# Kernel optimization log

Hardware: AMD Instinct MI355X
Metric: run time of the kernel (lower is better)

The kernel has to match this reference:

```python
import jax, jax.numpy as jnp
import numpy as np

NEAR_PLANE = 1e-4
MIN_COV = 1e-4
SIGMA_RADIUS = 3.0
ALPHA_MAX = 0.999  # clamp for numerical stability of log1p(-alpha)


def setup_inputs() -> dict:
    key = jax.random.key(0)
    k1, k2, k3, k4, k5 = jax.random.split(key, 5)
    N = 1024
    H = W = 192
    # Gaussians in front of an identity-pose camera
    xy = jax.random.uniform(k1, (N, 2), minval=-2.0, maxval=2.0)
    z = jax.random.uniform(k2, (N, 1), minval=1.0, maxval=8.0)
    means = jnp.concatenate([xy, z], axis=1).astype(jnp.float32)
    A = jax.random.normal(k3, (N, 3, 3), dtype=jnp.float32) * 0.05
    covariances = jnp.einsum('nij,nkj->nik', A, A) + 1e-4 * jnp.eye(3, dtype=jnp.float32)
    colors = jax.random.uniform(k4, (N, 3), dtype=jnp.float32)
    opacities = jax.random.uniform(k5, (N,), dtype=jnp.float32)
    fx = fy = 200.0
    intrinsics = jnp.array([[fx, 0.0, W / 2.0], [0.0, fy, H / 2.0], [0.0, 0.0, 1.0]], dtype=jnp.float32)
    camera_to_world = jnp.eye(4, dtype=jnp.float32)
    return {
        'means': means, 'covariances': covariances, 'colors': colors,
        'opacities': opacities, 'intrinsics': intrinsics,
        'camera_to_world': camera_to_world, 'height': H, 'width': W,
    }


def _render(means, covariances, colors, opacities, intrinsics, camera_to_world, height, width):
    # world -> camera
    R = camera_to_world[:3, :3].T                      # rotation_w2c
    t = -R @ camera_to_world[:3, 3]
    mc = means @ R.T + t                               # [N,3] camera-space means
    covc = jnp.einsum('ij,njk,lk->nil', R, covariances, R)  # [N,3,3]
    x, y, z = mc[:, 0], mc[:, 1], mc[:, 2]
    vis = z > NEAR_PLANE
    sz = jnp.where(vis, z, 1.0)
    fx, fy = intrinsics[0, 0], intrinsics[1, 1]
    cx, cy = intrinsics[0, 2], intrinsics[1, 2]
    mx = fx * x / sz + cx
    my = fy * y / sz + cy
    # projection Jacobian [N,2,3]
    zer = jnp.zeros_like(sz)
    J = jnp.stack([
        jnp.stack([fx / sz, zer, -fx * x / (sz * sz)], axis=-1),
        jnp.stack([zer, fy / sz, -fy * y / (sz * sz)], axis=-1),
    ], axis=1)
    cov2 = jnp.einsum('nij,njk,nlk->nil', J, covc, J) + MIN_COV * jnp.eye(2, dtype=means.dtype)
    a, b, c = cov2[:, 0, 0], cov2[:, 0, 1], cov2[:, 1, 1]
    # max eigenvalue -> support radius -> axis-aligned bbox
    disc = jnp.sqrt(jnp.clip((a - c) ** 2 + 4.0 * b * b, 0.0, None))
    lam = jnp.maximum(0.5 * (a + c + disc), MIN_COV)
    rad = SIGMA_RADIUS * jnp.sqrt(lam)
    min_x = jnp.floor(mx - rad); max_x = jnp.ceil(mx + rad)
    min_y = jnp.floor(my - rad); max_y = jnp.ceil(my + rad)
    overlap = vis & (max_x >= 0) & (min_x < width) & (max_y >= 0) & (min_y < height)
    # depth sort (culled Gaussians pushed to the back with alpha forced to 0)
    order = jnp.argsort(jnp.where(overlap, z, jnp.inf))
    mx, my = mx[order], my[order]
    a, b, c = a[order], b[order], c[order]
    min_x, max_x = min_x[order], max_x[order]
    min_y, max_y = min_y[order], max_y[order]
    op = jnp.where(overlap[order], opacities[order], 0.0)
    cols = colors[order]
    # inverse 2x2 covariance
    det = jnp.maximum(a * c - b * b, 1e-12)
    ia, ib, ic = c / det, -b / det, a / det
    xs = jnp.arange(width, dtype=mx.dtype)
    ys = jnp.arange(height, dtype=mx.dtype)
    dx = xs[None, None, :] - mx[:, None, None]         # [N,1,W]
    dy = ys[None, :, None] - my[:, None, None]         # [N,H,1]
    # Mahalanobis distance per (gaussian, pixel): [N,H,W]
    q = (ia[:, None, None] * dx * dx
         + 2.0 * ib[:, None, None] * dx * dy
         + ic[:, None, None] * dy * dy)
    w = jnp.exp(-0.5 * q)
    in_x = (xs[None, None, :] >= min_x[:, None, None]) & (xs[None, None, :] <= max_x[:, None, None])
    in_y = (ys[None, :, None] >= min_y[:, None, None]) & (ys[None, :, None] <= max_y[:, None, None])
    inside = (in_x & in_y).astype(w.dtype)
    alpha = jnp.clip(op[:, None, None] * w, 0.0, ALPHA_MAX) * inside  # [N,H,W]
    # front-to-back compositing: T_i = prod_{j<i}(1 - alpha_j), exclusive
    logc = jnp.cumsum(jnp.log1p(-alpha), axis=0)
    T = jnp.exp(jnp.concatenate([jnp.zeros_like(logc[:1]), logc[:-1]], axis=0))
    img = jnp.einsum('nhw,nc->hwc', alpha * T, cols)   # [H,W,3]
    return img


def reference(means, covariances, colors, opacities, intrinsics, camera_to_world, height, width):
    return _render(means, covariances, colors, opacities, intrinsics, camera_to_world, height, width)
```

## Files before the change

kernel.cpp:

```cpp
#include <hip/hip_runtime.h>
#include <stdint.h>
#include <math.h>

#define NEAR_PLANE 0.0001f
#define MIN_COV    0.0001f
#define SIGMA_RAD  3.0f
#define ALPHA_MAX  0.999f


__global__ __launch_bounds__(256) void gs_prep(
        const float* __restrict__ means,
        const float* __restrict__ covs,
        const float* __restrict__ colors,
        const float* __restrict__ opac,
        const float* __restrict__ K,
        const float* __restrict__ c2w,
        const int* __restrict__ hp, const int* __restrict__ wp,
        float4* __restrict__ params,
        unsigned* __restrict__ zb,
        uint2* __restrict__ bbox,
        int N) {
    int i = blockIdx.x * blockDim.x + threadIdx.x;
    if (i >= N) return;
    float Wf = (float)(*wp), Hf = (float)(*hp);

    float R[3][3];
    #pragma unroll
    for (int r = 0; r < 3; ++r)
        #pragma unroll
        for (int c = 0; c < 3; ++c)
            R[r][c] = c2w[c * 4 + r];
    float ct0 = c2w[3], ct1 = c2w[7], ct2 = c2w[11];
    float t0 = -(R[0][0]*ct0 + R[0][1]*ct1 + R[0][2]*ct2);
    float t1 = -(R[1][0]*ct0 + R[1][1]*ct1 + R[1][2]*ct2);
    float t2 = -(R[2][0]*ct0 + R[2][1]*ct1 + R[2][2]*ct2);

    float m0 = means[i*3+0], m1 = means[i*3+1], m2 = means[i*3+2];
    float x = R[0][0]*m0 + R[0][1]*m1 + R[0][2]*m2 + t0;
    float y = R[1][0]*m0 + R[1][1]*m1 + R[1][2]*m2 + t1;
    float z = R[2][0]*m0 + R[2][1]*m1 + R[2][2]*m2 + t2;

    const float* C = covs + i * 9;
    float M[3][3], CC[3][3];
    #pragma unroll
    for (int r = 0; r < 3; ++r)
        #pragma unroll
        for (int c = 0; c < 3; ++c)
            M[r][c] = R[r][0]*C[0*3+c] + R[r][1]*C[1*3+c] + R[r][2]*C[2*3+c];
    #pragma unroll
    for (int r = 0; r < 3; ++r)
        #pragma unroll
        for (int c = 0; c < 3; ++c)
            CC[r][c] = M[r][0]*R[c][0] + M[r][1]*R[c][1] + M[r][2]*R[c][2];

    bool vis = z > NEAR_PLANE;
    float sz = vis ? z : 1.0f;
    float fx = K[0], fy = K[4], cx = K[2], cy = K[5];
    float mx = fx * x / sz + cx;
    float my = fy * y / sz + cy;

    float a0 = fx / sz, a2 = -fx * x / (sz * sz);
    float b1 = fy / sz, b2 = -fy * y / (sz * sz);
    float u0 = a0*CC[0][0] + a2*CC[2][0];
    float u1 = a0*CC[0][1] + a2*CC[2][1];
    float u2 = a0*CC[0][2] + a2*CC[2][2];
    float v1 = b1*CC[1][1] + b2*CC[2][1];
    float v2 = b1*CC[1][2] + b2*CC[2][2];
    float a = u0*a0 + u2*a2 + MIN_COV;
    float b = u1*b1 + u2*b2;
    float c = v1*b1 + v2*b2 + MIN_COV;

    float disc = sqrtf(fmaxf((a - c)*(a - c) + 4.0f*b*b, 0.0f));
    float lam  = fmaxf(0.5f*(a + c + disc), MIN_COV);
    float rad  = SIGMA_RAD * sqrtf(lam);
    float minx = floorf(mx - rad), maxx = ceilf(mx + rad);
    float miny = floorf(my - rad), maxy = ceilf(my + rad);
    bool overlap = vis && (maxx >= 0.0f) && (minx < Wf) && (maxy >= 0.0f) && (miny < Hf);

    float det = fmaxf(a*c - b*b, 1e-12f);

    int mnx, mxx, mny, mxy;
    if (overlap) {
        mnx = (int)fmaxf(fminf(minx,  32767.0f), -32768.0f);
        mxx = (int)fmaxf(fminf(maxx,  32767.0f), -32768.0f);
        mny = (int)fmaxf(fminf(miny,  32767.0f), -32768.0f);
        mxy = (int)fmaxf(fminf(maxy,  32767.0f), -32768.0f);
    } else {
        mnx = 32767; mxx = -32768; mny = 32767; mxy = -32768;
    }
    float op = overlap ? opac[i] : 0.0f;
    params[i*3+0] = make_float4(mx, my, c / det, -b / det);
    params[i*3+1] = make_float4(a / det, op, colors[i*3+0], colors[i*3+1]);
    params[i*3+2] = make_float4(colors[i*3+2], 0.0f, 0.0f, 0.0f);

    zb[i] = overlap ? __float_as_uint(z) : 0x7F800000u;
    bbox[i] = make_uint2((unsigned)(mnx & 0xFFFF) | ((unsigned)(mxx & 0xFFFF) << 16),
                         (unsigned)(mny & 0xFFFF) | ((unsigned)(mxy & 0xFFFF) << 16));
}

__global__ __launch_bounds__(256) void gs_render(
        const float4* __restrict__ params,
        const unsigned* __restrict__ zb,
        const uint2* __restrict__ bbox,
        int W, int H, int N,
        float* __restrict__ out) {
    __shared__ unsigned long long sk[1024];
    __shared__ float4 sp[1024 * 3];
    __shared__ float4 s_part[4][64];
    __shared__ int s_cnt;

    int tid = threadIdx.x;
    int lane = tid & 63, wv = tid >> 6;
    int tilesX = (W + 7) >> 3;
    int tile = blockIdx.x;
    int tx0 = (tile % tilesX) << 3, ty0 = (tile / tilesX) << 3;
    int txMax = tx0 + 7, tyMax = ty0 + 7;

    if (tid == 0) s_cnt = 0;
    __syncthreads();

    for (int r = 0; r < N; r += 256) {
        int i = r + tid;
        bool keep = false;
        unsigned long long key = 0;
        if (i < N) {
            uint2 bb = bbox[i];
            int gmnx = ((int)bb.x << 16) >> 16, gmxx = (int)bb.x >> 16;
            int gmny = ((int)bb.y << 16) >> 16, gmxy = (int)bb.y >> 16;
            keep = (gmxx >= tx0) & (gmnx <= txMax) & (gmxy >= ty0) & (gmny <= tyMax);
            if (keep) key = ((unsigned long long)zb[i] << 32) | (unsigned)i;
        }
        unsigned long long m = __ballot(keep);
        int base = 0;
        if (lane == 0 && m) base = atomicAdd(&s_cnt, __popcll(m));
        base = __shfl(base, 0, 64);
        if (keep) {
            int pos = __popcll(m & ((1ull << lane) - 1ull));
            sk[base + pos] = key;
        }
    }
    __syncthreads();
    int S = s_cnt;

    int pad = 1;
    while (pad < S) pad <<= 1;
    for (int i = S + tid; i < pad; i += 256) sk[i] = ~0ull;
    __syncthreads();
    for (int k = 2; k <= pad; k <<= 1) {
        for (int j = k >> 1; j > 0; j >>= 1) {
            for (int i = tid; i < pad; i += 256) {
                int ixj = i ^ j;
                if (ixj > i) {
                    unsigned long long A = sk[i], B = sk[ixj];
                    bool up = (i & k) == 0;
                    if ((A > B) == up) { sk[i] = B; sk[ixj] = A; }
                }
            }
            __syncthreads();
        }
    }

    for (int i = tid; i < S; i += 256) {
        int g = (int)(sk[i] & 0xFFFFFFFFull);
        sp[i*3+0] = params[g*3+0];
        sp[i*3+1] = params[g*3+1];
        sp[i*3+2] = params[g*3+2];
    }
    __syncthreads();

    int per = (S + 3) >> 2;
    int lo = wv * per, hi = min(S, lo + per);
    int px = tx0 + (lane & 7), py = ty0 + (lane >> 3);
    float fpx = (float)px, fpy = (float)py;
    float T = 1.0f, accr = 0.0f, accg = 0.0f, accb = 0.0f;
    for (int i = lo; i < hi; ++i) {
        float4 l0 = sp[i*3+0];
        float4 l1 = sp[i*3+1];
        float  cb = sp[i*3+2].x;
        float dx = fpx - l0.x, dy = fpy - l0.y;
        float q = fmaf(l0.z * dx, dx, fmaf(2.0f * l0.w * dx, dy, l1.x * dy * dy));
        float w = __expf(-0.5f * q);
        float alpha = fminf(l1.y * w, ALPHA_MAX);
        float at = alpha * T;
        accr = fmaf(at, l1.z, accr);
        accg = fmaf(at, l1.w, accg);
        accb = fmaf(at, cb, accb);
        T = T - at;
        if (__all(T < 1e-6f)) break;
    }
    s_part[wv][lane] = make_float4(accr, accg, accb, T);
    __syncthreads();

    if (wv == 0 && px < W && py < H) {
        float Tc = 1.0f, r = 0.0f, g = 0.0f, b = 0.0f;
        #pragma unroll
        for (int s = 0; s < 4; ++s) {
            float4 p = s_part[s][lane];
            r = fmaf(Tc, p.x, r);
            g = fmaf(Tc, p.y, g);
            b = fmaf(Tc, p.z, b);
            Tc *= p.w;
        }
        int pix = py * W + px;
        out[pix*3+0] = r;
        out[pix*3+1] = g;
        out[pix*3+2] = b;
    }
}

extern "C" void kernel_launch(void* const* d_in, const int* in_sizes, int n_in,
                              void* d_out, int out_size, void* d_ws, size_t ws_size,
                              hipStream_t stream) {
    const float* means  = (const float*)d_in[0];
    const float* covs   = (const float*)d_in[1];
    const float* colors = (const float*)d_in[2];
    const float* opac   = (const float*)d_in[3];
    const float* K      = (const float*)d_in[4];
    const float* c2w    = (const float*)d_in[5];
    const int*   hp     = (const int*)d_in[6];
    const int*   wp     = (const int*)d_in[7];

    int N = in_sizes[0] / 3;
    int npix = out_size / 3;
    int W = (int)(sqrt((double)npix) + 0.5);
    int H = npix / W;

    char* ws = (char*)d_ws;
    float4*   params = (float4*)ws;
    unsigned* zbp    = (unsigned*)(ws + (size_t)N * 48);
    uint2*    bboxp  = (uint2*)(ws + (size_t)N * 52);

    gs_prep<<<(N + 255) / 256, 256, 0, stream>>>(means, covs, colors, opac, K, c2w,
                                                 hp, wp, params, zbp, bboxp, N);

    int tilesX = (W + 7) / 8, tilesY = (H + 7) / 8;
    gs_render<<<tilesX * tilesY, 256, 0, stream>>>(params, zbp, bboxp, W, H, N,
                                                   (float*)d_out);
}
```

Before: 23.77 us.

## Fuse projection into per-tile render kernel and sort small lists in registers

```diff
diff --git a/kernel.cpp b/kernel.cpp
--- a/kernel.cpp
+++ b/kernel.cpp
@@ -7,23 +7,39 @@
 #define SIGMA_RAD  3.0f
 #define ALPHA_MAX  0.999f
 
-
-__global__ __launch_bounds__(256) void gs_prep(
+__device__ inline unsigned long long shflx64(unsigned long long v, int j) {
+    int lo = __shfl_xor((int)(unsigned)(v & 0xFFFFFFFFull), j, 64);
+    int hi = __shfl_xor((int)(unsigned)(v >> 32), j, 64);
+    return ((unsigned long long)(unsigned)hi << 32) | (unsigned)lo;
+}
+
+__global__ __launch_bounds__(256) void gs_fused(
         const float* __restrict__ means,
         const float* __restrict__ covs,
         const float* __restrict__ colors,
         const float* __restrict__ opac,
         const float* __restrict__ K,
         const float* __restrict__ c2w,
-        const int* __restrict__ hp, const int* __restrict__ wp,
-        float4* __restrict__ params,
-        unsigned* __restrict__ zb,
-        uint2* __restrict__ bbox,
-        int N) {
-    int i = blockIdx.x * blockDim.x + threadIdx.x;
-    if (i >= N) return;
-    float Wf = (float)(*wp), Hf = (float)(*hp);
-
+        int W, int H, int N,
+        float* __restrict__ out) {
+    __shared__ float4 sp[1024 * 3];
+    __shared__ unsigned long long sk[1024];
+    __shared__ float4 s_aux[256];
+    __shared__ int s_cnt;
+
+    unsigned* szb = (unsigned*)s_aux;
+    float4 (*s_part)[64] = (float4 (*)[64])s_aux;
+
+    int tid = threadIdx.x;
+    int lane = tid & 63, wv = tid >> 6;
+    int tilesX = (W + 7) >> 3;
+    int tile = blockIdx.x;
+    int tx0 = (tile % tilesX) << 3, ty0 = (tile / tilesX) << 3;
+    int txMax = tx0 + 7, tyMax = ty0 + 7;
+
+    if (tid == 0) s_cnt = 0;
+
+    float Wf = (float)W, Hf = (float)H;
     float R[3][3];
     #pragma unroll
     for (int r = 0; r < 3; ++r)
@@ -34,101 +50,85 @@
     float t0 = -(R[0][0]*ct0 + R[0][1]*ct1 + R[0][2]*ct2);
     float t1 = -(R[1][0]*ct0 + R[1][1]*ct1 + R[1][2]*ct2);
     float t2 = -(R[2][0]*ct0 + R[2][1]*ct1 + R[2][2]*ct2);
-
-    float m0 = means[i*3+0], m1 = means[i*3+1], m2 = means[i*3+2];
-    float x = R[0][0]*m0 + R[0][1]*m1 + R[0][2]*m2 + t0;
-    float y = R[1][0]*m0 + R[1][1]*m1 + R[1][2]*m2 + t1;
-    float z = R[2][0]*m0 + R[2][1]*m1 + R[2][2]*m2 + t2;
-
-    const float* C = covs + i * 9;
-    float M[3][3], CC[3][3];
-    #pragma unroll
-    for (int r = 0; r < 3; ++r)
-        #pragma unroll
-        for (int c = 0; c < 3; ++c)
-            M[r][c] = R[r][0]*C[0*3+c] + R[r][1]*C[1*3+c] + R[r][2]*C[2*3+c];
-    #pragma unroll
-    for (int r = 0; r < 3; ++r)
-        #pragma unroll
-        for (int c = 0; c < 3; ++c)
-            CC[r][c] = M[r][0]*R[c][0] + M[r][1]*R[c][1] + M[r][2]*R[c][2];
-
-    bool vis = z > NEAR_PLANE;
-    float sz = vis ? z : 1.0f;
     float fx = K[0], fy = K[4], cx = K[2], cy = K[5];
-    float mx = fx * x / sz + cx;
-    float my = fy * y / sz + cy;
-
-    float a0 = fx / sz, a2 = -fx * x / (sz * sz);
-    float b1 = fy / sz, b2 = -fy * y / (sz * sz);
-    float u0 = a0*CC[0][0] + a2*CC[2][0];
-    float u1 = a0*CC[0][1] + a2*CC[2][1];
-    float u2 = a0*CC[0][2] + a2*CC[2][2];
-    float v1 = b1*CC[1][1] + b2*CC[2][1];
-    float v2 = b1*CC[1][2] + b2*CC[2][2];
-    float a = u0*a0 + u2*a2 + MIN_COV;
-    float b = u1*b1 + u2*b2;
-    float c = v1*b1 + v2*b2 + MIN_COV;
-
-    float disc = sqrtf(fmaxf((a - c)*(a - c) + 4.0f*b*b, 0.0f));
-    float lam  = fmaxf(0.5f*(a + c + disc), MIN_COV);
-    float rad  = SIGMA_RAD * sqrtf(lam);
-    float minx = floorf(mx - rad), maxx = ceilf(mx + rad);
-    float miny = floorf(my - rad), maxy = ceilf(my + rad);
-    bool overlap = vis && (maxx >= 0.0f) && (minx < Wf) && (maxy >= 0.0f) && (miny < Hf);
-
-    float det = fmaxf(a*c - b*b, 1e-12f);
-
-    int mnx, mxx, mny, mxy;
-    if (overlap) {
-        mnx = (int)fmaxf(fminf(minx,  32767.0f), -32768.0f);
-        mxx = (int)fmaxf(fminf(maxx,  32767.0f), -32768.0f);
-        mny = (int)fmaxf(fminf(miny,  32767.0f), -32768.0f);
-        mxy = (int)fmaxf(fminf(maxy,  32767.0f), -32768.0f);
-    } else {
-        mnx = 32767; mxx = -32768; mny = 32767; mxy = -32768;
-    }
-    float op = overlap ? opac[i] : 0.0f;
-    params[i*3+0] = make_float4(mx, my, c / det, -b / det);
-    params[i*3+1] = make_float4(a / det, op, colors[i*3+0], colors[i*3+1]);
-    params[i*3+2] = make_float4(colors[i*3+2], 0.0f, 0.0f, 0.0f);
-
-    zb[i] = overlap ? __float_as_uint(z) : 0x7F800000u;
-    bbox[i] = make_uint2((unsigned)(mnx & 0xFFFF) | ((unsigned)(mxx & 0xFFFF) << 16),
-                         (unsigned)(mny & 0xFFFF) | ((unsigned)(mxy & 0xFFFF) << 16));
-}
-
-__global__ __launch_bounds__(256) void gs_render(
-        const float4* __restrict__ params,
-        const unsigned* __restrict__ zb,
-        const uint2* __restrict__ bbox,
-        int W, int H, int N,
-        float* __restrict__ out) {
-    __shared__ unsigned long long sk[1024];
-    __shared__ float4 sp[1024 * 3];
-    __shared__ float4 s_part[4][64];
-    __shared__ int s_cnt;
-
-    int tid = threadIdx.x;
-    int lane = tid & 63, wv = tid >> 6;
-    int tilesX = (W + 7) >> 3;
-    int tile = blockIdx.x;
-    int tx0 = (tile % tilesX) << 3, ty0 = (tile / tilesX) << 3;
-    int txMax = tx0 + 7, tyMax = ty0 + 7;
-
-    if (tid == 0) s_cnt = 0;
-    __syncthreads();
-
-    for (int r = 0; r < N; r += 256) {
-        int i = r + tid;
+
+    #pragma unroll 4
+    for (int i = tid; i < N; i += 256) {
+        float m0 = means[i*3+0], m1 = means[i*3+1], m2 = means[i*3+2];
+        float x = R[0][0]*m0 + R[0][1]*m1 + R[0][2]*m2 + t0;
+        float y = R[1][0]*m0 + R[1][1]*m1 + R[1][2]*m2 + t1;
+        float z = R[2][0]*m0 + R[2][1]*m1 + R[2][2]*m2 + t2;
+
+        const float* C = covs + i * 9;
+        float M[3][3], CC[3][3];
+        #pragma unroll
+        for (int r = 0; r < 3; ++r)
+            #pragma unroll
+            for (int c = 0; c < 3; ++c)
+                M[r][c] = R[r][0]*C[0*3+c] + R[r][1]*C[1*3+c] + R[r][2]*C[2*3+c];
+        #pragma unroll
+        for (int r = 0; r < 3; ++r)
+            #pragma unroll
+            for (int c = 0; c < 3; ++c)
+                CC[r][c] = M[r][0]*R[c][0] + M[r][1]*R[c][1] + M[r][2]*R[c][2];
+
+        bool vis = z > NEAR_PLANE;
+        float sz = vis ? z : 1.0f;
+        float mx = fx * x / sz + cx;
+        float my = fy * y / sz + cy;
+
+        float a0 = fx / sz, a2 = -fx * x / (sz * sz);
+        float b1 = fy / sz, b2 = -fy * y / (sz * sz);
+        float u0 = a0*CC[0][0] + a2*CC[2][0];
+        float u1 = a0*CC[0][1] + a2*CC[2][1];
+        float u2 = a0*CC[0][2] + a2*CC[2][2];
+        float v1 = b1*CC[1][1] + b2*CC[2][1];
+        float v2 = b1*CC[1][2] + b2*CC[2][2];
+        float a = u0*a0 + u2*a2 + MIN_COV;
+        float b = u1*b1 + u2*b2;
+        float c = v1*b1 + v2*b2 + MIN_COV;
+
+        float disc = sqrtf(fmaxf((a - c)*(a - c) + 4.0f*b*b, 0.0f));
+        float lam  = fmaxf(0.5f*(a + c + disc), MIN_COV);
+        float rad  = SIGMA_RAD * sqrtf(lam);
+        float minx = floorf(mx - rad), maxx = ceilf(mx + rad);
+        float miny = floorf(my - rad), maxy = ceilf(my + rad);
+        bool overlap = vis && (maxx >= 0.0f) && (minx < Wf) && (maxy >= 0.0f) && (miny < Hf);
+
+        float det = fmaxf(a*c - b*b, 1e-12f);
+
+        int mnx, mxx, mny, mxy;
+        if (overlap) {
+            mnx = (int)fmaxf(fminf(minx,  32767.0f), -32768.0f);
+            mxx = (int)fmaxf(fminf(maxx,  32767.0f), -32768.0f);
+            mny = (int)fmaxf(fminf(miny,  32767.0f), -32768.0f);
+            mxy = (int)fmaxf(fminf(maxy,  32767.0f), -32768.0f);
+        } else {
+            mnx = 32767; mxx = -32768; mny = 32767; mxy = -32768;
+        }
+        unsigned p01 = (unsigned)(mnx & 0xFFFF) | ((unsigned)(mxx & 0xFFFF) << 16);
+        unsigned p23 = (unsigned)(mny & 0xFFFF) | ((unsigned)(mxy & 0xFFFF) << 16);
+        float op = overlap ? opac[i] : 0.0f;
+
+        sp[i*3+0] = make_float4(mx, my, c / det, -b / det);
+        sp[i*3+1] = make_float4(a / det, op, colors[i*3+0], colors[i*3+1]);
+        sp[i*3+2] = make_float4(__int_as_float((int)p01), __int_as_float((int)p23),
+                                colors[i*3+2], 0.0f);
+        szb[i] = overlap ? __float_as_uint(z) : 0x7F800000u;
+    }
+    __syncthreads();
+
+    for (int rr = 0; rr < N; rr += 256) {
+        int i = rr + tid;
         bool keep = false;
         unsigned long long key = 0;
         if (i < N) {
-            uint2 bb = bbox[i];
-            int gmnx = ((int)bb.x << 16) >> 16, gmxx = (int)bb.x >> 16;
-            int gmny = ((int)bb.y << 16) >> 16, gmxy = (int)bb.y >> 16;
+            float4 v2r = sp[i*3+2];
+            int bb01 = __float_as_int(v2r.x), bb23 = __float_as_int(v2r.y);
+            int gmnx = (bb01 << 16) >> 16, gmxx = bb01 >> 16;
+            int gmny = (bb23 << 16) >> 16, gmxy = bb23 >> 16;
             keep = (gmxx >= tx0) & (gmnx <= txMax) & (gmxy >= ty0) & (gmny <= tyMax);
-            if (keep) key = ((unsigned long long)zb[i] << 32) | (unsigned)i;
+            if (keep) key = ((unsigned long long)szb[i] << 32) | (unsigned)i;
         }
         unsigned long long m = __ballot(keep);
         int base = 0;
@@ -144,29 +144,47 @@
 
     int pad = 1;
     while (pad < S) pad <<= 1;
-    for (int i = S + tid; i < pad; i += 256) sk[i] = ~0ull;
-    __syncthreads();
-    for (int k = 2; k <= pad; k <<= 1) {
-        for (int j = k >> 1; j > 0; j >>= 1) {
-            for (int i = tid; i < pad; i += 256) {
-                int ixj = i ^ j;
-                if (ixj > i) {
-                    unsigned long long A = sk[i], B = sk[ixj];
-                    bool up = (i & k) == 0;
-                    if ((A > B) == up) { sk[i] = B; sk[ixj] = A; }
+
+    if (pad <= 256) {
+        int v = tid;
+        unsigned long long key = (v < S) ? sk[v] : ~0ull;
+        for (int k = 2; k <= pad; k <<= 1) {
+            for (int j = k >> 1; j > 0; j >>= 1) {
+                if (j >= 64) {
+                    if (v < pad) sk[v] = key;
+                    __syncthreads();
+                    unsigned long long p = (v < pad) ? sk[v ^ j] : 0;
+                    __syncthreads();
+                    if (v < pad) {
+                        bool tm = (((v & j) == 0) == ((v & k) == 0));
+                        key = (tm == (key < p)) ? key : p;
+                    }
+                } else {
+                    unsigned long long p = shflx64(key, j);
+                    bool tm = (((v & j) == 0) == ((v & k) == 0));
+                    key = (tm == (key < p)) ? key : p;
                 }
             }
-            __syncthreads();
-        }
-    }
-
-    for (int i = tid; i < S; i += 256) {
-        int g = (int)(sk[i] & 0xFFFFFFFFull);
-        sp[i*3+0] = params[g*3+0];
-        sp[i*3+1] = params[g*3+1];
-        sp[i*3+2] = params[g*3+2];
-    }
-    __syncthreads();
+        }
+        if (v < pad) sk[v] = key;
+        __syncthreads();
+    } else {
+        for (int i = S + tid; i < pad; i += 256) sk[i] = ~0ull;
+        __syncthreads();
+        for (int k = 2; k <= pad; k <<= 1) {
+            for (int j = k >> 1; j > 0; j >>= 1) {
+                for (int i = tid; i < pad; i += 256) {
+                    int ixj = i ^ j;
+                    if (ixj > i) {
+                        unsigned long long A = sk[i], B = sk[ixj];
+                        bool up = (i & k) == 0;
+                        if ((A > B) == up) { sk[i] = B; sk[ixj] = A; }
+                    }
+                }
+                __syncthreads();
+            }
+        }
+    }
 
     int per = (S + 3) >> 2;
     int lo = wv * per, hi = min(S, lo + per);
@@ -174,20 +192,25 @@
     float fpx = (float)px, fpy = (float)py;
     float T = 1.0f, accr = 0.0f, accg = 0.0f, accb = 0.0f;
     for (int i = lo; i < hi; ++i) {
-        float4 l0 = sp[i*3+0];
-        float4 l1 = sp[i*3+1];
-        float  cb = sp[i*3+2].x;
+        int g = (int)(sk[i] & 0xFFFFFFFFull);
+        float4 l0 = sp[g*3+0];
+        float4 l1 = sp[g*3+1];
+        float4 l2 = sp[g*3+2];
+        int b01 = __float_as_int(l2.x), b23 = __float_as_int(l2.y);
+        bool inside = (px >= ((b01 << 16) >> 16)) & (px <= (b01 >> 16))
+                    & (py >= ((b23 << 16) >> 16)) & (py <= (b23 >> 16));
         float dx = fpx - l0.x, dy = fpy - l0.y;
         float q = fmaf(l0.z * dx, dx, fmaf(2.0f * l0.w * dx, dy, l1.x * dy * dy));
         float w = __expf(-0.5f * q);
-        float alpha = fminf(l1.y * w, ALPHA_MAX);
+        float alpha = inside ? fminf(l1.y * w, ALPHA_MAX) : 0.0f;
         float at = alpha * T;
         accr = fmaf(at, l1.z, accr);
         accg = fmaf(at, l1.w, accg);
-        accb = fmaf(at, cb, accb);
+        accb = fmaf(at, l2.z, accb);
         T = T - at;
         if (__all(T < 1e-6f)) break;
     }
+    __syncthreads();
     s_part[wv][lane] = make_float4(accr, accg, accb, T);
     __syncthreads();
 
@@ -217,23 +240,13 @@
     const float* opac   = (const float*)d_in[3];
     const float* K      = (const float*)d_in[4];
     const float* c2w    = (const float*)d_in[5];
-    const int*   hp     = (const int*)d_in[6];
-    const int*   wp     = (const int*)d_in[7];
 
     int N = in_sizes[0] / 3;
     int npix = out_size / 3;
     int W = (int)(sqrt((double)npix) + 0.5);
     int H = npix / W;
 
-    char* ws = (char*)d_ws;
-    float4*   params = (float4*)ws;
-    unsigned* zbp    = (unsigned*)(ws + (size_t)N * 48);
-    uint2*    bboxp  = (uint2*)(ws + (size_t)N * 52);
-
-    gs_prep<<<(N + 255) / 256, 256, 0, stream>>>(means, covs, colors, opac, K, c2w,
-                                                 hp, wp, params, zbp, bboxp, N);
-
     int tilesX = (W + 7) / 8, tilesY = (H + 7) / 8;
-    gs_render<<<tilesX * tilesY, 256, 0, stream>>>(params, zbp, bboxp, W, H, N,
-                                                   (float*)d_out);
+    gs_fused<<<tilesX * tilesY, 256, 0, stream>>>(means, covs, colors, opac, K, c2w,
+                                                  W, H, N, (float*)d_out);
 }
```

After: 23.89 us. About the same (+0.5%).

## Sort gaussians once globally by depth instead of per-tile bitonic sort

Applied to the files above, without the earlier changes.

```diff
diff --git a/kernel.cpp b/kernel.cpp
--- a/kernel.cpp
+++ b/kernel.cpp
@@ -7,6 +7,11 @@
 #define SIGMA_RAD  3.0f
 #define ALPHA_MAX  0.999f
 
+__device__ inline unsigned long long shflx64(unsigned long long v, int j) {
+    int lo = __shfl_xor((int)(unsigned)(v & 0xFFFFFFFFull), j, 64);
+    int hi = __shfl_xor((int)(unsigned)(v >> 32), j, 64);
+    return ((unsigned long long)(unsigned)hi << 32) | (unsigned)lo;
+}
 
 __global__ __launch_bounds__(256) void gs_prep(
         const float* __restrict__ means,
@@ -88,26 +93,52 @@
     } else {
         mnx = 32767; mxx = -32768; mny = 32767; mxy = -32768;
     }
+    unsigned p01 = (unsigned)(mnx & 0xFFFF) | ((unsigned)(mxx & 0xFFFF) << 16);
+    unsigned p23 = (unsigned)(mny & 0xFFFF) | ((unsigned)(mxy & 0xFFFF) << 16);
     float op = overlap ? opac[i] : 0.0f;
+
     params[i*3+0] = make_float4(mx, my, c / det, -b / det);
     params[i*3+1] = make_float4(a / det, op, colors[i*3+0], colors[i*3+1]);
-    params[i*3+2] = make_float4(colors[i*3+2], 0.0f, 0.0f, 0.0f);
-
+    params[i*3+2] = make_float4(__int_as_float((int)p01), __int_as_float((int)p23),
+                                colors[i*3+2], 0.0f);
     zb[i] = overlap ? __float_as_uint(z) : 0x7F800000u;
-    bbox[i] = make_uint2((unsigned)(mnx & 0xFFFF) | ((unsigned)(mxx & 0xFFFF) << 16),
-                         (unsigned)(mny & 0xFFFF) | ((unsigned)(mxy & 0xFFFF) << 16));
+    bbox[i] = make_uint2(p01, p23);
+}
+
+__global__ __launch_bounds__(1024) void gs_sort(
+        const unsigned* __restrict__ zb,
+        int* __restrict__ perm, int N) {
+    __shared__ unsigned long long sk[1024];
+    int i = threadIdx.x;
+    unsigned long long key = ((unsigned long long)zb[i] << 32) | (unsigned)i;
+    for (int k = 2; k <= N; k <<= 1) {
+        int j = k >> 1;
+        for (; j >= 64; j >>= 1) {
+            sk[i] = key;
+            __syncthreads();
+            unsigned long long p = sk[i ^ j];
+            __syncthreads();
+            bool tm = (((i & j) == 0) == ((i & k) == 0));
+            key = (tm == (key < p)) ? key : p;
+        }
+        for (; j >= 1; j >>= 1) {
+            unsigned long long p = shflx64(key, j);
+            bool tm = (((i & j) == 0) == ((i & k) == 0));
+            key = (tm == (key < p)) ? key : p;
+        }
+    }
+    perm[i] = (int)(key & 0xFFFFFFFFull);
 }
 
 __global__ __launch_bounds__(256) void gs_render(
         const float4* __restrict__ params,
-        const unsigned* __restrict__ zb,
         const uint2* __restrict__ bbox,
+        const int* __restrict__ perm,
         int W, int H, int N,
         float* __restrict__ out) {
-    __shared__ unsigned long long sk[1024];
-    __shared__ float4 sp[1024 * 3];
+    __shared__ int s_surv[1024];
+    __shared__ int s_wcnt[4];
     __shared__ float4 s_part[4][64];
-    __shared__ int s_cnt;
 
     int tid = threadIdx.x;
     int lane = tid & 63, wv = tid >> 6;
@@ -116,75 +147,58 @@
     int tx0 = (tile % tilesX) << 3, ty0 = (tile / tilesX) << 3;
     int txMax = tx0 + 7, tyMax = ty0 + 7;
 
-    if (tid == 0) s_cnt = 0;
-    __syncthreads();
-
-    for (int r = 0; r < N; r += 256) {
-        int i = r + tid;
+    int running = 0;
+    for (int rr = 0; rr < N; rr += 256) {
+        int i = rr + tid;
         bool keep = false;
-        unsigned long long key = 0;
+        int g = 0;
         if (i < N) {
-            uint2 bb = bbox[i];
+            g = perm[i];
+            uint2 bb = bbox[g];
             int gmnx = ((int)bb.x << 16) >> 16, gmxx = (int)bb.x >> 16;
             int gmny = ((int)bb.y << 16) >> 16, gmxy = (int)bb.y >> 16;
             keep = (gmxx >= tx0) & (gmnx <= txMax) & (gmxy >= ty0) & (gmny <= tyMax);
-            if (keep) key = ((unsigned long long)zb[i] << 32) | (unsigned)i;
         }
         unsigned long long m = __ballot(keep);
-        int base = 0;
-        if (lane == 0 && m) base = atomicAdd(&s_cnt, __popcll(m));
-        base = __shfl(base, 0, 64);
+        if (lane == 0) s_wcnt[wv] = __popcll(m);
+        __syncthreads();
+        int base = running;
+        #pragma unroll
+        for (int w = 0; w < 4; ++w) {
+            int cw = s_wcnt[w];
+            if (w < wv) base += cw;
+            running += cw;
+        }
         if (keep) {
             int pos = __popcll(m & ((1ull << lane) - 1ull));
-            sk[base + pos] = key;
-        }
-    }
-    __syncthreads();
-    int S = s_cnt;
-
-    int pad = 1;
-    while (pad < S) pad <<= 1;
-    for (int i = S + tid; i < pad; i += 256) sk[i] = ~0ull;
-    __syncthreads();
-    for (int k = 2; k <= pad; k <<= 1) {
-        for (int j = k >> 1; j > 0; j >>= 1) {
-            for (int i = tid; i < pad; i += 256) {
-                int ixj = i ^ j;
-                if (ixj > i) {
-                    unsigned long long A = sk[i], B = sk[ixj];
-                    bool up = (i & k) == 0;
-                    if ((A > B) == up) { sk[i] = B; sk[ixj] = A; }
-                }
-            }
-            __syncthreads();
-        }
-    }
-
-    for (int i = tid; i < S; i += 256) {
-        int g = (int)(sk[i] & 0xFFFFFFFFull);
-        sp[i*3+0] = params[g*3+0];
-        sp[i*3+1] = params[g*3+1];
-        sp[i*3+2] = params[g*3+2];
-    }
-    __syncthreads();
+            s_surv[base + pos] = g;
+        }
+        __syncthreads();
+    }
+    int S = running;
 
     int per = (S + 3) >> 2;
     int lo = wv * per, hi = min(S, lo + per);
     int px = tx0 + (lane & 7), py = ty0 + (lane >> 3);
     float fpx = (float)px, fpy = (float)py;
     float T = 1.0f, accr = 0.0f, accg = 0.0f, accb = 0.0f;
+    #pragma unroll 2
     for (int i = lo; i < hi; ++i) {
-        float4 l0 = sp[i*3+0];
-        float4 l1 = sp[i*3+1];
-        float  cb = sp[i*3+2].x;
+        int g = s_surv[i];
+        float4 l0 = params[g*3+0];
+        float4 l1 = params[g*3+1];
+        float4 l2 = params[g*3+2];
+        int b01 = __float_as_int(l2.x), b23 = __float_as_int(l2.y);
+        bool inside = (px >= ((b01 << 16) >> 16)) & (px <= (b01 >> 16))
+                    & (py >= ((b23 << 16) >> 16)) & (py <= (b23 >> 16));
         float dx = fpx - l0.x, dy = fpy - l0.y;
         float q = fmaf(l0.z * dx, dx, fmaf(2.0f * l0.w * dx, dy, l1.x * dy * dy));
         float w = __expf(-0.5f * q);
-        float alpha = fminf(l1.y * w, ALPHA_MAX);
+        float alpha = inside ? fminf(l1.y * w, ALPHA_MAX) : 0.0f;
         float at = alpha * T;
         accr = fmaf(at, l1.z, accr);
         accg = fmaf(at, l1.w, accg);
-        accb = fmaf(at, cb, accb);
+        accb = fmaf(at, l2.z, accb);
         T = T - at;
         if (__all(T < 1e-6f)) break;
     }
@@ -229,11 +243,13 @@
     float4*   params = (float4*)ws;
     unsigned* zbp    = (unsigned*)(ws + (size_t)N * 48);
     uint2*    bboxp  = (uint2*)(ws + (size_t)N * 52);
+    int*      perm   = (int*)(ws + (size_t)N * 60);
 
     gs_prep<<<(N + 255) / 256, 256, 0, stream>>>(means, covs, colors, opac, K, c2w,
                                                  hp, wp, params, zbp, bboxp, N);
+    gs_sort<<<1, N, 0, stream>>>(zbp, perm, N);
 
     int tilesX = (W + 7) / 8, tilesY = (H + 7) / 8;
-    gs_render<<<tilesX * tilesY, 256, 0, stream>>>(params, zbp, bboxp, W, H, N,
+    gs_render<<<tilesX * tilesY, 256, 0, stream>>>(params, bboxp, perm, W, H, N,
                                                    (float*)d_out);
 }
```

New measurement: 26.27 us. +10.5%, slower.

## Use register bitonic sort with shuffles and read params directly from global memory

Applied to the files above, without the earlier changes.

```diff
diff --git a/kernel.cpp b/kernel.cpp
--- a/kernel.cpp
+++ b/kernel.cpp
@@ -7,6 +7,11 @@
 #define SIGMA_RAD  3.0f
 #define ALPHA_MAX  0.999f
 
+__device__ inline unsigned long long shflx64(unsigned long long v, int j) {
+    int lo = __shfl_xor((int)(unsigned)(v & 0xFFFFFFFFull), j, 64);
+    int hi = __shfl_xor((int)(unsigned)(v >> 32), j, 64);
+    return ((unsigned long long)(unsigned)hi << 32) | (unsigned)lo;
+}
 
 __global__ __launch_bounds__(256) void gs_prep(
         const float* __restrict__ means,
@@ -88,14 +93,16 @@
     } else {
         mnx = 32767; mxx = -32768; mny = 32767; mxy = -32768;
     }
+    unsigned p01 = (unsigned)(mnx & 0xFFFF) | ((unsigned)(mxx & 0xFFFF) << 16);
+    unsigned p23 = (unsigned)(mny & 0xFFFF) | ((unsigned)(mxy & 0xFFFF) << 16);
     float op = overlap ? opac[i] : 0.0f;
+
     params[i*3+0] = make_float4(mx, my, c / det, -b / det);
     params[i*3+1] = make_float4(a / det, op, colors[i*3+0], colors[i*3+1]);
-    params[i*3+2] = make_float4(colors[i*3+2], 0.0f, 0.0f, 0.0f);
-
+    params[i*3+2] = make_float4(__int_as_float((int)p01), __int_as_float((int)p23),
+                                colors[i*3+2], 0.0f);
     zb[i] = overlap ? __float_as_uint(z) : 0x7F800000u;
-    bbox[i] = make_uint2((unsigned)(mnx & 0xFFFF) | ((unsigned)(mxx & 0xFFFF) << 16),
-                         (unsigned)(mny & 0xFFFF) | ((unsigned)(mxy & 0xFFFF) << 16));
+    bbox[i] = make_uint2(p01, p23);
 }
 
 __global__ __launch_bounds__(256) void gs_render(
@@ -105,7 +112,6 @@
         int W, int H, int N,
         float* __restrict__ out) {
     __shared__ unsigned long long sk[1024];
-    __shared__ float4 sp[1024 * 3];
     __shared__ float4 s_part[4][64];
     __shared__ int s_cnt;
 
@@ -119,8 +125,8 @@
     if (tid == 0) s_cnt = 0;
     __syncthreads();
 
-    for (int r = 0; r < N; r += 256) {
-        int i = r + tid;
+    for (int rr = 0; rr < N; rr += 256) {
+        int i = rr + tid;
         bool keep = false;
         unsigned long long key = 0;
         if (i < N) {
@@ -144,47 +150,70 @@
 
     int pad = 1;
     while (pad < S) pad <<= 1;
-    for (int i = S + tid; i < pad; i += 256) sk[i] = ~0ull;
-    __syncthreads();
-    for (int k = 2; k <= pad; k <<= 1) {
-        for (int j = k >> 1; j > 0; j >>= 1) {
-            for (int i = tid; i < pad; i += 256) {
-                int ixj = i ^ j;
-                if (ixj > i) {
-                    unsigned long long A = sk[i], B = sk[ixj];
-                    bool up = (i & k) == 0;
-                    if ((A > B) == up) { sk[i] = B; sk[ixj] = A; }
+
+    if (pad <= 256) {
+        int v = tid;
+        unsigned long long key = (v < S) ? sk[v] : ~0ull;
+        for (int k = 2; k <= pad; k <<= 1) {
+            for (int j = k >> 1; j > 0; j >>= 1) {
+                if (j >= 64) {
+                    if (v < pad) sk[v] = key;
+                    __syncthreads();
+                    unsigned long long p = (v < pad) ? sk[v ^ j] : 0;
+                    __syncthreads();
+                    if (v < pad) {
+                        bool tm = (((v & j) == 0) == ((v & k) == 0));
+                        key = (tm == (key < p)) ? key : p;
+                    }
+                } else {
+                    unsigned long long p = shflx64(key, j);
+                    bool tm = (((v & j) == 0) == ((v & k) == 0));
+                    key = (tm == (key < p)) ? key : p;
                 }
             }
-            __syncthreads();
-        }
-    }
-
-    for (int i = tid; i < S; i += 256) {
-        int g = (int)(sk[i] & 0xFFFFFFFFull);
-        sp[i*3+0] = params[g*3+0];
-        sp[i*3+1] = params[g*3+1];
-        sp[i*3+2] = params[g*3+2];
-    }
-    __syncthreads();
+        }
+        if (v < pad) sk[v] = key;
+        __syncthreads();
+    } else {
+        for (int i = S + tid; i < pad; i += 256) sk[i] = ~0ull;
+        __syncthreads();
+        for (int k = 2; k <= pad; k <<= 1) {
+            for (int j = k >> 1; j > 0; j >>= 1) {
+                for (int i = tid; i < pad; i += 256) {
+                    int ixj = i ^ j;
+                    if (ixj > i) {
+                        unsigned long long A = sk[i], B = sk[ixj];
+                        bool up = (i & k) == 0;
+                        if ((A > B) == up) { sk[i] = B; sk[ixj] = A; }
+                    }
+                }
+                __syncthreads();
+            }
+        }
+    }
 
     int per = (S + 3) >> 2;
     int lo = wv * per, hi = min(S, lo + per);
     int px = tx0 + (lane & 7), py = ty0 + (lane >> 3);
     float fpx = (float)px, fpy = (float)py;
     float T = 1.0f, accr = 0.0f, accg = 0.0f, accb = 0.0f;
+    #pragma unroll 2
     for (int i = lo; i < hi; ++i) {
-        float4 l0 = sp[i*3+0];
-        float4 l1 = sp[i*3+1];
-        float  cb = sp[i*3+2].x;
+        int g = (int)(sk[i] & 0xFFFFFFFFull);
+        float4 l0 = params[g*3+0];
+        float4 l1 = params[g*3+1];
+        float4 l2 = params[g*3+2];
+        int b01 = __float_as_int(l2.x), b23 = __float_as_int(l2.y);
+        bool inside = (px >= ((b01 << 16) >> 16)) & (px <= (b01 >> 16))
+                    & (py >= ((b23 << 16) >> 16)) & (py <= (b23 >> 16));
         float dx = fpx - l0.x, dy = fpy - l0.y;
         float q = fmaf(l0.z * dx, dx, fmaf(2.0f * l0.w * dx, dy, l1.x * dy * dy));
         float w = __expf(-0.5f * q);
-        float alpha = fminf(l1.y * w, ALPHA_MAX);
+        float alpha = inside ? fminf(l1.y * w, ALPHA_MAX) : 0.0f;
         float at = alpha * T;
         accr = fmaf(at, l1.z, accr);
         accg = fmaf(at, l1.w, accg);
-        accb = fmaf(at, cb, accb);
+        accb = fmaf(at, l2.z, accb);
         T = T - at;
         if (__all(T < 1e-6f)) break;
     }
```

Result: faster. 20.46 us (-13.9%).
